# Performance work log

Measured on AMD Instinct MI355X. Metric: run time of the kernel, lower is better.

## Reference

```python
import jax, jax.numpy as jnp
import numpy as np

B, T, DM, H, D, BT = 4, 2048, 1024, 16, 64, 16
ETA_BASE = 0.01
LN_EPS = 1e-05
THETA = 10000.0


def _ln(x, w, b):
    # x: (B,H,t,D); per-head LayerNorm over last dim, w/b: (H,D)
    mu = x.mean(-1, keepdims=True)
    var = x.var(-1, keepdims=True)
    xhat = (x - mu) * jax.lax.rsqrt(var + LN_EPS)
    return xhat * w[None, :, None, :] + b[None, :, None, :]


def _ln_bwd(x, g, w):
    # gradient of LayerNorm wrt input x given upstream grad g on the output
    mu = x.mean(-1, keepdims=True)
    var = x.var(-1, keepdims=True)
    inv = jax.lax.rsqrt(var + LN_EPS)
    xhat = (x - mu) * inv
    dxhat = g * w[None, :, None, :]
    return (dxhat - dxhat.mean(-1, keepdims=True) - xhat * (dxhat * xhat).mean(-1, keepdims=True)) * inv


def _rope(q, k):
    # standard rotate-half RoPE, start_pos = 0
    pos = jnp.arange(T, dtype=jnp.float32)
    inv_freq = 1.0 / (THETA ** (jnp.arange(0, D, 2, dtype=jnp.float32) / D))
    freqs = pos[:, None] * inv_freq[None, :]            # (T, D/2)
    emb = jnp.concatenate([freqs, freqs], axis=-1)      # (T, D)
    cos = jnp.cos(emb)[None, None]                      # (1,1,T,D)
    sin = jnp.sin(emb)[None, None]

    def rot(x):
        x1, x2 = jnp.split(x, 2, axis=-1)
        return jnp.concatenate([-x2, x1], axis=-1)

    return q * cos + rot(q) * sin, k * cos + rot(k) * sin


def _forward(x, W, Wq, Wk, Wv, Wo, Wlr, ln_w, ln_b):
    def shape(y):
        return y.reshape(B, T, H, D).transpose(0, 2, 1, 3)  # (B,H,T,D)

    q = shape(x @ Wq.T)
    k = shape(x @ Wk.T)
    v = shape(x @ Wv.T)
    q, k = _rope(q, k)

    # lr gating: eta = eta_base * sigmoid(theta_lr(x)), shared across heads
    eta = ETA_BASE * jax.nn.sigmoid(x @ Wlr.T)          # (B,T,1)
    eta = jnp.broadcast_to(eta, (B, T, H)).transpose(0, 2, 1)  # (B,H,T)

    nc = T // BT

    def chunks(a):
        return a.reshape(B, H, nc, BT, D).transpose(2, 0, 1, 3, 4)  # (nc,B,H,BT,D)

    Kc, Vc, Qc = chunks(k), chunks(v), chunks(q)
    Ec = eta.reshape(B, H, nc, BT).transpose(2, 0, 1, 3)            # (nc,B,H,BT)
    mask = jnp.tril(jnp.ones((BT, BT), dtype=bool), -1)              # strict lower

    def step(Wst, inp):
        Kb, Vb, Qb, Eb = inp
        tK = jnp.einsum('bhtd,bhed->bhte', Kb, Wst)                  # K @ W^T
        g = (2.0 / BT) * (Kb + _ln(tK, ln_w, ln_b) - Vb)
        u = _ln_bwd(tK, g, ln_w)
        S = jnp.einsum('bhtd,bhsd->bhts', Qb, Kb)
        Ue = u * Eb[..., None]
        corr = jnp.einsum('bhts,bhse->bhte', jnp.where(mask, S, 0.0), Ue)
        TQ = jnp.einsum('bhtd,bhed->bhte', Qb, Wst) - corr
        Z = Qb + _ln(TQ, ln_w, ln_b)
        Wn = Wst - jnp.einsum('bhti,bhtj->bhij', Ue, Kb)
        return Wn, Z

    Wf, Zc = jax.lax.scan(step, W, (Kc, Vc, Qc, Ec))
    # (nc,B,H,BT,D) -> (B,T,H*D)
    z = Zc.transpose(1, 2, 0, 3, 4).reshape(B, H, T, D).transpose(0, 2, 1, 3).reshape(B, T, H * D)
    return z @ Wo.T, Wf


def setup_inputs() -> dict:
    key = jax.random.key(0)
    ks = jax.random.split(key, 9)
    return {
        'x': jax.random.normal(ks[0], (B, T, DM), dtype=jnp.float32),
        'W': 0.02 * jax.random.normal(ks[1], (B, H, D, D), dtype=jnp.float32),
        'Wq': 0.02 * jax.random.normal(ks[2], (DM, DM), dtype=jnp.float32),
        'Wk': 0.02 * jax.random.normal(ks[3], (DM, DM), dtype=jnp.float32),
        'Wv': 0.02 * jax.random.normal(ks[4], (DM, DM), dtype=jnp.float32),
        'Wo': 0.02 * jax.random.normal(ks[5], (DM, DM), dtype=jnp.float32),
        'Wlr': 0.02 * jax.random.normal(ks[6], (1, DM), dtype=jnp.float32),
        'ln_w': jnp.ones((H, D), dtype=jnp.float32),
        'ln_b': jnp.zeros((H, D), dtype=jnp.float32),
    }


def reference(x, W, Wq, Wk, Wv, Wo, Wlr, ln_w, ln_b):
    return _forward(x, W, Wq, Wk, Wv, Wo, Wlr, ln_w, ln_b)
```

## Files before the change

kernel.cpp:

```cpp
#include <hip/hip_runtime.h>
#include <math.h>

#define B_ 4
#define T_ 2048
#define DM_ 1024
#define H_ 16
#define D_ 64
#define BT_ 16
#define NC_ 128

typedef _Float16 half8 __attribute__((ext_vector_type(8)));
typedef _Float16 half4 __attribute__((ext_vector_type(4)));
typedef float f32x4 __attribute__((ext_vector_type(4)));

#define MFMA16 __builtin_amdgcn_mfma_f32_16x16x32_f16

__device__ __forceinline__ void stage16(const _Float16* g, _Float16* l) {
  __builtin_amdgcn_global_load_lds(
      (const __attribute__((address_space(1))) unsigned int*)(const void*)g,
      (__attribute__((address_space(3))) unsigned int*)(void*)l, 16, 0, 0);
}

template <int CTRL>
__device__ __forceinline__ float dppadd(float x) {
  return x + __int_as_float(__builtin_amdgcn_update_dpp(0, __float_as_int(x), CTRL, 0xf, 0xf, true));
}
__device__ __forceinline__ float wrs(float v) {
  v = dppadd<0x111>(v);
  v = dppadd<0x112>(v);
  v = dppadd<0x114>(v);
  v = dppadd<0x118>(v);
  v = dppadd<0x142>(v);
  v = dppadd<0x143>(v);
  return __int_as_float(__builtin_amdgcn_readlane(__float_as_int(v), 63));
}

__device__ __forceinline__ int sw128(int row, int slot) {
  return row * 128 + ((slot ^ (row & 7)) * 16);
}

__global__ void k_rope_table(float* __restrict__ cosT, float* __restrict__ sinT) {
  int idx = blockIdx.x * blockDim.x + threadIdx.x;
  if (idx >= T_ * 32) return;
  int t = idx >> 5, i = idx & 31;
  float inv = powf(10000.0f, -((float)(2 * i)) / 64.0f);
  float f = (float)t * inv;
  cosT[idx] = cosf(f);
  sinT[idx] = sinf(f);
}

__global__ __launch_bounds__(256) void k_eta(const float* __restrict__ x,
                                             const float* __restrict__ Wlr,
                                             float* __restrict__ eta) {
  int w = threadIdx.x >> 6, l = threadIdx.x & 63;
  int row = blockIdx.x * 4 + w;
  const float* xr = x + (size_t)row * DM_;
  float s = 0.f;
#pragma unroll
  for (int j = 0; j < DM_ / 64; ++j) s += xr[j * 64 + l] * Wlr[j * 64 + l];
  s = wrs(s);
  if (l == 0) eta[row] = 0.01f / (1.0f + expf(-s));
}

__global__ __launch_bounds__(256) void k_cvt(const float* __restrict__ x,
                                             const float* __restrict__ Wq,
                                             const float* __restrict__ Wk,
                                             const float* __restrict__ Wv,
                                             const float* __restrict__ Wo,
                                             _Float16* __restrict__ xh,
                                             _Float16* __restrict__ wh) {
  int gid = blockIdx.x * 256 + threadIdx.x;
  const float* src;
  _Float16* dst;
  size_t off;
  if (gid < 1048576) {
    src = x; dst = xh; off = (size_t)gid * 8;
  } else {
    int j = gid - 1048576;
    int sel = j >> 17, jj = j & 131071;
    src = (sel == 0) ? Wq : (sel == 1) ? Wk : (sel == 2) ? Wv : Wo;
    dst = wh + (size_t)sel * 1048576;
    off = (size_t)jj * 8;
  }
  float4 a = *(const float4*)&src[off];
  float4 b = *(const float4*)&src[off + 4];
  half8 h;
  h[0] = (_Float16)a.x; h[1] = (_Float16)a.y; h[2] = (_Float16)a.z; h[3] = (_Float16)a.w;
  h[4] = (_Float16)b.x; h[5] = (_Float16)b.y; h[6] = (_Float16)b.z; h[7] = (_Float16)b.w;
  *(half8*)&dst[off] = h;
}

__global__ __launch_bounds__(256) void k_gemm_qkv_h(const _Float16* __restrict__ xh,
                                                    const _Float16* __restrict__ wh,
                                                    const float* __restrict__ cosT,
                                                    const float* __restrict__ sinT,
                                                    _Float16* __restrict__ qo,
                                                    _Float16* __restrict__ ko,
                                                    _Float16* __restrict__ vo) {
  __shared__ __align__(16) union {
    _Float16 ab[2][128 * 64];
    _Float16 ep[128][136];
  } sm;
  _Float16* As = sm.ab[0];
  _Float16* Bs = sm.ab[1];
  int tid = threadIdx.x;
  int m0 = blockIdx.x * 128;
  int by = blockIdx.y;
  int mat = by >> 3;
  int n0 = (by & 7) * 128;
  const _Float16* Bsrc = wh + (size_t)mat * 1048576;
  _Float16* op = (mat == 0) ? qo : (mat == 1) ? ko : vo;
  int wid = tid >> 6, l = tid & 63;
  int m0w = (wid >> 1) * 64, n0w = (wid & 1) * 64;
  int l15 = l & 15, l4 = l >> 4;

  f32x4 acc[4][4];
#pragma unroll
  for (int i = 0; i < 4; ++i)
#pragma unroll
    for (int j = 0; j < 4; ++j) acc[i][j] = (f32x4){0.f, 0.f, 0.f, 0.f};

  int srow_in = l >> 3;
  int schunk_l = l & 7;
  for (int k0 = 0; k0 < 1024; k0 += 64) {
#pragma unroll
    for (int i = 0; i < 4; ++i) {
      int row = wid * 32 + i * 8 + srow_in;
      int sc = schunk_l ^ (row & 7);
      stage16(xh + (size_t)(m0 + row) * 1024 + k0 + sc * 8, As + (wid * 32 + i * 8) * 64);
      stage16(Bsrc + (size_t)(n0 + row) * 1024 + k0 + sc * 8, Bs + (wid * 32 + i * 8) * 64);
    }
    __syncthreads();
#pragma unroll
    for (int kk = 0; kk < 2; ++kk) {
      half8 a[4], b[4];
#pragma unroll
      for (int mi = 0; mi < 4; ++mi) {
        int row = m0w + mi * 16 + l15;
        a[mi] = *(half8*)((char*)As + sw128(row, kk * 4 + l4));
      }
#pragma unroll
      for (int ni = 0; ni < 4; ++ni) {
        int row = n0w + ni * 16 + l15;
        b[ni] = *(half8*)((char*)Bs + sw128(row, kk * 4 + l4));
      }
#pragma unroll
      for (int mi = 0; mi < 4; ++mi)
#pragma unroll
        for (int ni = 0; ni < 4; ++ni)
          acc[mi][ni] = MFMA16(a[mi], b[ni], acc[mi][ni], 0, 0, 0);
    }
    __syncthreads();
  }

  if (mat < 2) {
#pragma unroll
    for (int mi = 0; mi < 4; ++mi)
#pragma unroll
      for (int r = 0; r < 4; ++r) {
        int m = m0 + m0w + mi * 16 + l4 * 4 + r;
        int t = m & (T_ - 1);
#pragma unroll
        for (int ni = 0; ni < 2; ++ni) {
          int d1 = ni * 16 + l15;
          float cv = cosT[t * 32 + d1];
          float sv = sinT[t * 32 + d1];
          float x1 = acc[mi][ni][r], x2 = acc[mi][ni + 2][r];
          acc[mi][ni][r] = x1 * cv - x2 * sv;
          acc[mi][ni + 2][r] = x2 * cv + x1 * sv;
        }
      }
  }

#pragma unroll
  for (int mi = 0; mi < 4; ++mi)
#pragma unroll
    for (int ni = 0; ni < 4; ++ni)
#pragma unroll
      for (int r = 0; r < 4; ++r) {
        int mrow = m0w + mi * 16 + l4 * 4 + r;
        int ncol = n0w + ni * 16 + l15;
        sm.ep[mrow][ncol] = (_Float16)acc[mi][ni][r];
      }
  __syncthreads();
  int bb = m0 >> 11, t0 = m0 & (T_ - 1);
#pragma unroll
  for (int seg = 0; seg < 2; ++seg) {
    int h0 = (by & 7) * 2 + seg;
    _Float16* dsth = op + ((size_t)(bb * H_ + h0) * T_ + t0) * D_;
#pragma unroll
    for (int p = 0; p < 4; ++p) {
      int idx = p * 256 + tid;
      int mrow = idx >> 3, c = idx & 7;
      half8 hv = *(half8*)&sm.ep[mrow][seg * 64 + c * 8];
      *(half8*)&dsth[mrow * 64 + c * 8] = hv;
    }
  }
}

__global__ __launch_bounds__(256) void k_gemm_out_h(const _Float16* __restrict__ zh,
                                                    const _Float16* __restrict__ woh,
                                                    float* __restrict__ out) {
  __shared__ __align__(16) union {
    _Float16 ab[2][128 * 64];
    float epf[64][132];
  } sm;
  _Float16* As = sm.ab[0];
  _Float16* Bs = sm.ab[1];
  int tid = threadIdx.x;
  int m0 = blockIdx.x * 128;
  int n0 = blockIdx.y * 128;
  int wid = tid >> 6, l = tid & 63;
  int m0w = (wid >> 1) * 64, n0w = (wid & 1) * 64;
  int l15 = l & 15, l4 = l >> 4;

  f32x4 acc[4][4];
#pragma unroll
  for (int i = 0; i < 4; ++i)
#pragma unroll
    for (int j = 0; j < 4; ++j) acc[i][j] = (f32x4){0.f, 0.f, 0.f, 0.f};

  int srow_in = l >> 3;
  int schunk_l = l & 7;
  for (int k0 = 0; k0 < 1024; k0 += 64) {
#pragma unroll
    for (int i = 0; i < 4; ++i) {
      int row = wid * 32 + i * 8 + srow_in;
      int sc = schunk_l ^ (row & 7);
      stage16(zh + (size_t)(m0 + row) * 1024 + k0 + sc * 8, As + (wid * 32 + i * 8) * 64);
      stage16(woh + (size_t)(n0 + row) * 1024 + k0 + sc * 8, Bs + (wid * 32 + i * 8) * 64);
    }
    __syncthreads();
#pragma unroll
    for (int kk = 0; kk < 2; ++kk) {
      half8 a[4], b[4];
#pragma unroll
      for (int mi = 0; mi < 4; ++mi) {
        int row = m0w + mi * 16 + l15;
        a[mi] = *(half8*)((char*)As + sw128(row, kk * 4 + l4));
      }
#pragma unroll
      for (int ni = 0; ni < 4; ++ni) {
        int row = n0w + ni * 16 + l15;
        b[ni] = *(half8*)((char*)Bs + sw128(row, kk * 4 + l4));
      }
#pragma unroll
      for (int mi = 0; mi < 4; ++mi)
#pragma unroll
        for (int ni = 0; ni < 4; ++ni)
          acc[mi][ni] = MFMA16(a[mi], b[ni], acc[mi][ni], 0, 0, 0);
    }
    __syncthreads();
  }

#pragma unroll
  for (int hi = 0; hi < 2; ++hi) {
    if ((wid >> 1) == hi) {
#pragma unroll
      for (int mi = 0; mi < 4; ++mi)
#pragma unroll
        for (int ni = 0; ni < 4; ++ni)
#pragma unroll
          for (int r = 0; r < 4; ++r)
            sm.epf[mi * 16 + l4 * 4 + r][n0w + ni * 16 + l15] = acc[mi][ni][r];
    }
    __syncthreads();
#pragma unroll
    for (int p = 0; p < 8; ++p) {
      int idx = p * 256 + tid;
      int mrow = idx >> 5, c = idx & 31;
      float4 v = *(float4*)&sm.epf[mrow][c * 4];
      *(float4*)&out[(size_t)(m0 + hi * 64 + mrow) * DM_ + n0 + c * 4] = v;
    }
    __syncthreads();
  }
}

__global__ __launch_bounds__(512) void k_scan(const _Float16* __restrict__ qg,
                                              const _Float16* __restrict__ kg,
                                              const _Float16* __restrict__ vg,
                                              const float* __restrict__ etag,
                                              const float* __restrict__ W0,
                                              const float* __restrict__ lnw_g,
                                              const float* __restrict__ lnb_g,
                                              _Float16* __restrict__ zg,
                                              float* __restrict__ wf) {
  __shared__ __align__(16) float Ksf[2][16][68], Qsf[2][16][68], Vsf[2][16][68];
  __shared__ __align__(16) _Float16 Ks_h[2][1024], Qs_h[2][1024];
  __shared__ __align__(16) _Float16 KT_h[2][64 * 24];
  __shared__ __align__(16) _Float16 Wh[64 * 64];
  __shared__ __align__(16) float tKs[16][68], tqs[16][68];
  __shared__ __align__(16) _Float16 Ss_h[16 * 24];
  __shared__ __align__(16) _Float16 UeT_h[64 * 24];
  __shared__ float Es[2][16];

  int bh = blockIdx.x, b = bh >> 4, h = bh & 15;
  int tid = threadIdx.x, w = tid >> 6, l = tid & 63;
  int l15 = l & 15, g = l >> 4;
  int ti = w >> 1, tj0 = (w & 1) * 2, tj1 = tj0 + 1;
  int d0 = tj0 * 16 + l15, d1 = tj1 * 16 + l15;

  float lw = lnw_g[h * 64 + l];
  float lb = lnb_g[h * 64 + l];
  const _Float16* kb = kg + (size_t)bh * (T_ * D_);
  const _Float16* qb = qg + (size_t)bh * (T_ * D_);
  const _Float16* vb = vg + (size_t)bh * (T_ * D_);

  const float* w0p = W0 + (size_t)bh * 4096;
  f32x4 accW0, accW1;
#pragma unroll
  for (int r = 0; r < 4; ++r) {
    int e = ti * 16 + g * 4 + r;
    accW0[r] = w0p[e * 64 + d0];
    accW1[r] = w0p[e * 64 + d1];
  }
#pragma unroll
  for (int r = 0; r < 4; ++r) {
    int e = ti * 16 + g * 4 + r;
    *(_Float16*)((char*)Wh + sw128(e, d0 >> 3) + (d0 & 7) * 2) = (_Float16)accW0[r];
    *(_Float16*)((char*)Wh + sw128(e, d1 >> 3) + (d1 & 7) * 2) = (_Float16)accW1[r];
  }

  {
    if (tid < 256) {
      int r = tid >> 4, c4 = (tid & 15) * 4;
      half4 fk = *(const half4*)&kb[r * 64 + c4];
      half4 fv = *(const half4*)&vb[r * 64 + c4];
#pragma unroll
      for (int i = 0; i < 4; ++i) {
        Ksf[0][r][c4 + i] = (float)fk[i];
        Vsf[0][r][c4 + i] = (float)fv[i];
        *(_Float16*)((char*)KT_h[0] + (c4 + i) * 48 + r * 2) = (_Float16)(-(float)fk[i]);
      }
      *(half4*)((char*)Ks_h[0] + sw128(r, c4 >> 3) + (c4 & 7) * 2) = fk;
      if (tid < 16) Es[0][tid] = etag[b * T_ + tid];
    } else {
      int t2 = tid - 256;
      int r = t2 >> 4, c4 = (t2 & 15) * 4;
      half4 fq = *(const half4*)&qb[r * 64 + c4];
#pragma unroll
      for (int i = 0; i < 4; ++i) Qsf[0][r][c4 + i] = (float)fq[i];
      *(half4*)((char*)Qs_h[0] + sw128(r, c4 >> 3) + (c4 & 7) * 2) = fq;
    }
  }

  const half8 Z8 = {0, 0, 0, 0, 0, 0, 0, 0};

  for (int c = 0; c < NC_; ++c) {
    int cur = c & 1, nxt = cur ^ 1;
    __syncthreads();

    bool pf = (c + 1 < NC_);
    half4 fk, fv, fq;
    float fe = 0.f;
    if (pf) {
      int goff = (c + 1) * (BT_ * D_);
      if (tid < 256) {
        int r = tid >> 4, c4 = (tid & 15) * 4;
        fk = *(const half4*)&kb[goff + r * 64 + c4];
        fv = *(const half4*)&vb[goff + r * 64 + c4];
        if (tid < 16) fe = etag[b * T_ + (c + 1) * BT_ + tid];
      } else {
        int t2 = tid - 256;
        int r = t2 >> 4, c4 = (t2 & 15) * 4;
        fq = *(const half4*)&qb[goff + r * 64 + c4];
      }
    }

    int j = w & 3;
    const _Float16* Asrc = (w < 4) ? Ks_h[cur] : Qs_h[cur];
    half8 a0 = *(const half8*)((const char*)Asrc + sw128(l15, g));
    half8 a1 = *(const half8*)((const char*)Asrc + sw128(l15, 4 + g));
    int ecol = j * 16 + l15;
    half8 b0 = *(const half8*)((const char*)Wh + sw128(ecol, g));
    half8 b1 = *(const half8*)((const char*)Wh + sw128(ecol, 4 + g));
    f32x4 accA = (f32x4){0.f, 0.f, 0.f, 0.f};
    accA = MFMA16(a0, b0, accA, 0, 0, 0);
    accA = MFMA16(a1, b1, accA, 0, 0, 0);
    if (w < 4) {
#pragma unroll
      for (int r = 0; r < 4; ++r) tKs[g * 4 + r][j * 16 + l15] = accA[r];
    } else if (w == 4) {
      f32x4 accS = (f32x4){0.f, 0.f, 0.f, 0.f};
      half8 kb0 = *(const half8*)((const char*)Ks_h[cur] + sw128(l15, g));
      half8 kb1 = *(const half8*)((const char*)Ks_h[cur] + sw128(l15, 4 + g));
      accS = MFMA16(a0, kb0, accS, 0, 0, 0);
      accS = MFMA16(a1, kb1, accS, 0, 0, 0);
#pragma unroll
      for (int r = 0; r < 4; ++r) {
        int t = g * 4 + r;
        Ss_h[t * 24 + l15] = (l15 < t) ? (_Float16)(-accS[r]) : (_Float16)0.f;
      }
    }
    __syncthreads();

#pragma unroll
    for (int i = 0; i < 2; ++i) {
      int t = i * 8 + w;
      float tkv = tKs[t][l];
      float s1 = wrs(tkv);
      float s2 = wrs(tkv * tkv);
      float mu = s1 * 0.015625f;
      float var = s2 * 0.015625f - mu * mu;
      float inv = rsqrtf(var + 1e-5f);
      float xhat = (tkv - mu) * inv;
      float ln = xhat * lw + lb;
      float gg = 0.125f * (Ksf[cur][t][l] + ln - Vsf[cur][t][l]);
      float dxh = gg * lw;
      float m1 = wrs(dxh) * 0.015625f;
      float m2 = wrs(dxh * xhat) * 0.015625f;
      float ue = (dxh - m1 - xhat * m2) * inv * Es[cur][t];
      UeT_h[l * 24 + t] = (_Float16)ue;
    }
    __syncthreads();

    if (w >= 4) {
      half8 as = Z8, bu = Z8;
      if (g < 2) {
        as = *(const half8*)((const char*)Ss_h + l15 * 48 + g * 16);
        bu = *(const half8*)((const char*)UeT_h + ((w - 4) * 16 + l15) * 48 + g * 16);
      }
      accA = MFMA16(as, bu, accA, 0, 0, 0);
#pragma unroll
      for (int r = 0; r < 4; ++r) tqs[g * 4 + r][(w - 4) * 16 + l15] = accA[r];
    }
    {
      half8 au = Z8, bk0 = Z8, bk1 = Z8;
      if (g < 2) {
        au = *(const half8*)((const char*)UeT_h + (ti * 16 + l15) * 48 + g * 16);
        bk0 = *(const half8*)((const char*)KT_h[cur] + (tj0 * 16 + l15) * 48 + g * 16);
        bk1 = *(const half8*)((const char*)KT_h[cur] + (tj1 * 16 + l15) * 48 + g * 16);
      }
      accW0 = MFMA16(au, bk0, accW0, 0, 0, 0);
      accW1 = MFMA16(au, bk1, accW1, 0, 0, 0);
#pragma unroll
      for (int r = 0; r < 4; ++r) {
        int e = ti * 16 + g * 4 + r;
        *(_Float16*)((char*)Wh + sw128(e, d0 >> 3) + (d0 & 7) * 2) = (_Float16)accW0[r];
        *(_Float16*)((char*)Wh + sw128(e, d1 >> 3) + (d1 & 7) * 2) = (_Float16)accW1[r];
      }
    }
    __syncthreads();

#pragma unroll
    for (int i = 0; i < 2; ++i) {
      int t = i * 8 + w;
      float tq = tqs[t][l];
      float s1 = wrs(tq);
      float s2 = wrs(tq * tq);
      float mu = s1 * 0.015625f;
      float var = s2 * 0.015625f - mu * mu;
      float inv = rsqrtf(var + 1e-5f);
      float zv = Qsf[cur][t][l] + ((tq - mu) * inv) * lw + lb;
      zg[((size_t)(b * T_ + c * BT_ + t)) * DM_ + h * 64 + l] = (_Float16)zv;
    }
    if (pf) {
      if (tid < 256) {
        int r = tid >> 4, c4 = (tid & 15) * 4;
#pragma unroll
        for (int i = 0; i < 4; ++i) {
          Ksf[nxt][r][c4 + i] = (float)fk[i];
          Vsf[nxt][r][c4 + i] = (float)fv[i];
          *(_Float16*)((char*)KT_h[nxt] + (c4 + i) * 48 + r * 2) = (_Float16)(-(float)fk[i]);
        }
        *(half4*)((char*)Ks_h[nxt] + sw128(r, c4 >> 3) + (c4 & 7) * 2) = fk;
        if (tid < 16) Es[nxt][tid] = fe;
      } else {
        int t2 = tid - 256;
        int r = t2 >> 4, c4 = (t2 & 15) * 4;
#pragma unroll
        for (int i = 0; i < 4; ++i) Qsf[nxt][r][c4 + i] = (float)fq[i];
        *(half4*)((char*)Qs_h[nxt] + sw128(r, c4 >> 3) + (c4 & 7) * 2) = fq;
      }
    }
  }

#pragma unroll
  for (int r = 0; r < 4; ++r) {
    int e = ti * 16 + g * 4 + r;
    wf[(size_t)bh * 4096 + e * 64 + d0] = accW0[r];
    wf[(size_t)bh * 4096 + e * 64 + d1] = accW1[r];
  }
}

extern "C" void kernel_launch(void* const* d_in, const int* in_sizes, int n_in,
                              void* d_out, int out_size, void* d_ws, size_t ws_size,
                              hipStream_t stream) {
  const float* x   = (const float*)d_in[0];
  const float* W0  = (const float*)d_in[1];
  const float* Wq  = (const float*)d_in[2];
  const float* Wk  = (const float*)d_in[3];
  const float* Wv  = (const float*)d_in[4];
  const float* Wo  = (const float*)d_in[5];
  const float* Wlr = (const float*)d_in[6];
  const float* lnw = (const float*)d_in[7];
  const float* lnb = (const float*)d_in[8];
  float* out = (float*)d_out;
  float* ws = (float*)d_ws;

  float* eta  = ws;
  float* cosT = eta + 8192;
  float* sinT = cosT + 65536;
  _Float16* q  = (_Float16*)(sinT + 65536);
  _Float16* k  = q + 8388608;
  _Float16* v  = k + 8388608;
  _Float16* xh = v + 8388608;
  _Float16* wh = xh + 8388608;
  _Float16* zh = xh;
  float* wf = out + 8388608;

  hipLaunchKernelGGL(k_rope_table, dim3(256), dim3(256), 0, stream, cosT, sinT);
  hipLaunchKernelGGL(k_cvt, dim3(6144), dim3(256), 0, stream, x, Wq, Wk, Wv, Wo, xh, wh);
  hipLaunchKernelGGL(k_eta, dim3(2048), dim3(256), 0, stream, x, Wlr, eta);
  hipLaunchKernelGGL(k_gemm_qkv_h, dim3(64, 24), dim3(256), 0, stream, xh, wh, cosT, sinT, q, k, v);
  hipLaunchKernelGGL(k_scan, dim3(64), dim3(512), 0, stream, q, k, v, eta, W0, lnw, lnb, zh, wf);
  hipLaunchKernelGGL(k_gemm_out_h, dim3(64, 8), dim3(256), 0, stream, zh, wh + 3145728, out);
}
```

Measured before the change: 426.5 us.

## Specialize scan warps into K/W-update and Q-output groups with skewed pipeline

Restructures the sequential chunk scan so warps 0-3 own the W state and the K-side gradient path, while warps 4-7 handle the Q path. The Q output's final MFMA, LayerNorm and store are deferred by one chunk so they overlap the next chunk's K-side work, cutting per-chunk barriers from four to three. Next-chunk K/Q tiles are prefetched with global_load_lds into swizzled, double-buffered LDS, and the fp32 K/Q/V LDS copies are replaced by per-thread register loads. This adds an epilogue for the last chunk, more LDS double buffers, and a less balanced work split between the warp groups.

```diff
diff --git a/kernel.cpp b/kernel.cpp
--- a/kernel.cpp
+++ b/kernel.cpp
@@ -37,6 +37,9 @@
 
 __device__ __forceinline__ int sw128(int row, int slot) {
   return row * 128 + ((slot ^ (row & 7)) * 16);
+}
+__device__ __forceinline__ int p64(int row, int slot) {
+  return row * 64 + ((slot ^ ((row >> 1) & 3)) * 16);
 }
 
 __global__ void k_rope_table(float* __restrict__ cosT, float* __restrict__ sinT) {
@@ -285,20 +288,18 @@
                                               const float* __restrict__ lnb_g,
                                               _Float16* __restrict__ zg,
                                               float* __restrict__ wf) {
-  __shared__ __align__(16) float Ksf[2][16][68], Qsf[2][16][68], Vsf[2][16][68];
-  __shared__ __align__(16) _Float16 Ks_h[2][1024], Qs_h[2][1024];
-  __shared__ __align__(16) _Float16 KT_h[2][64 * 24];
-  __shared__ __align__(16) _Float16 Wh[64 * 64];
-  __shared__ __align__(16) float tKs[16][68], tqs[16][68];
-  __shared__ __align__(16) _Float16 Ss_h[16 * 24];
-  __shared__ __align__(16) _Float16 UeT_h[64 * 24];
-  __shared__ float Es[2][16];
+  __shared__ __align__(16) _Float16 Wh[4096];
+  __shared__ __align__(16) _Float16 Kh[2][1024];
+  __shared__ __align__(16) _Float16 Qh[2][1024];
+  __shared__ __align__(16) _Float16 KTl[2][2048];
+  __shared__ __align__(16) _Float16 UeTl[2][2048];
+  __shared__ __align__(16) _Float16 Ssl[2][512];
+  __shared__ float tKs[16][68];
+  __shared__ float tqs[16][68];
 
   int bh = blockIdx.x, b = bh >> 4, h = bh & 15;
   int tid = threadIdx.x, w = tid >> 6, l = tid & 63;
-  int l15 = l & 15, g = l >> 4;
-  int ti = w >> 1, tj0 = (w & 1) * 2, tj1 = tj0 + 1;
-  int d0 = tj0 * 16 + l15, d1 = tj1 * 16 + l15;
+  int l15 = l & 15, g = l >> 4, u = w - 4;
 
   float lw = lnw_g[h * 64 + l];
   float lb = lnb_g[h * 64 + l];
@@ -306,180 +307,222 @@
   const _Float16* qb = qg + (size_t)bh * (T_ * D_);
   const _Float16* vb = vg + (size_t)bh * (T_ * D_);
 
-  const float* w0p = W0 + (size_t)bh * 4096;
-  f32x4 accW0, accW1;
-#pragma unroll
-  for (int r = 0; r < 4; ++r) {
-    int e = ti * 16 + g * 4 + r;
-    accW0[r] = w0p[e * 64 + d0];
-    accW1[r] = w0p[e * 64 + d1];
-  }
-#pragma unroll
-  for (int r = 0; r < 4; ++r) {
-    int e = ti * 16 + g * 4 + r;
-    *(_Float16*)((char*)Wh + sw128(e, d0 >> 3) + (d0 & 7) * 2) = (_Float16)accW0[r];
-    *(_Float16*)((char*)Wh + sw128(e, d1 >> 3) + (d1 & 7) * 2) = (_Float16)accW1[r];
-  }
-
+  f32x4 accW[4];
+  f32x4 accQ = (f32x4){0.f, 0.f, 0.f, 0.f};
+
+  if (w < 4) {
+    const float* w0p = W0 + (size_t)bh * 4096;
+#pragma unroll
+    for (int dt = 0; dt < 4; ++dt)
+#pragma unroll
+      for (int r = 0; r < 4; ++r)
+        accW[dt][r] = w0p[(w * 16 + g * 4 + r) * 64 + dt * 16 + l15];
+#pragma unroll
+    for (int dt = 0; dt < 4; ++dt)
+#pragma unroll
+      for (int r = 0; r < 4; ++r) {
+        int e = w * 16 + g * 4 + r, d = dt * 16 + l15;
+        *(_Float16*)((char*)Wh + e * 128 + (((d >> 3) ^ (e & 7)) * 16) + (d & 7) * 2) =
+            (_Float16)accW[dt][r];
+      }
+  }
+  for (int i = tid; i < 4096; i += 512) {
+    ((_Float16*)KTl)[i] = (_Float16)0.f;
+    ((_Float16*)UeTl)[i] = (_Float16)0.f;
+  }
+  for (int i = tid; i < 1024; i += 512) ((_Float16*)Ssl)[i] = (_Float16)0.f;
+  __syncthreads();
+
+  if (w >= 4) {
+    const _Float16* src = (w < 6) ? kb : qb;
+    _Float16* dst = (w < 6) ? Kh[0] : Qh[0];
+    int hf = w & 1, row = hf * 8 + (l >> 3), ch = (l & 7) ^ (row & 7);
+    stage16(src + row * 64 + ch * 8, dst + hf * 512);
+    if (w == 4) {
+      half8 ka = *(const half8*)(kb + (l & 15) * 64 + (l >> 4) * 16);
+      half8 ka2 = *(const half8*)(kb + (l & 15) * 64 + (l >> 4) * 16 + 8);
+#pragma unroll
+      for (int i = 0; i < 16; ++i) {
+        float v = (float)((i < 8) ? ka[i] : ka2[i - 8]);
+        int d = (l >> 4) * 16 + i, t = l & 15;
+        *(_Float16*)((char*)KTl[0] + d * 64 + ((((t >> 3)) ^ ((d >> 1) & 3)) * 16) + (t & 7) * 2) =
+            (_Float16)(-v);
+      }
+    }
+  }
+
+  float kf[4], vf[4], et[4], qf[4];
+#pragma unroll
+  for (int i = 0; i < 4; ++i) { kf[i] = vf[i] = et[i] = qf[i] = 0.f; }
+
+  for (int c = 0; c < NC_; ++c) {
+    int cb = c & 1, p = cb ^ 1;
+    __syncthreads();
+
+    if (w < 4) {
+#pragma unroll
+      for (int i = 0; i < 4; ++i) {
+        int t = i * 4 + w;
+        kf[i] = (float)kb[c * 1024 + t * 64 + l];
+        vf[i] = (float)vb[c * 1024 + t * 64 + l];
+        et[i] = etag[b * T_ + c * BT_ + t];
+      }
+      half8 bw0 = *(half8*)((char*)Wh + sw128(w * 16 + l15, g));
+      half8 bw1 = *(half8*)((char*)Wh + sw128(w * 16 + l15, 4 + g));
+      half8 ak0 = *(half8*)((char*)Kh[cb] + sw128(l15, g));
+      half8 ak1 = *(half8*)((char*)Kh[cb] + sw128(l15, 4 + g));
+      f32x4 a = (f32x4){0.f, 0.f, 0.f, 0.f};
+      a = MFMA16(ak0, bw0, a, 0, 0, 0);
+      a = MFMA16(ak1, bw1, a, 0, 0, 0);
+#pragma unroll
+      for (int r = 0; r < 4; ++r) tKs[g * 4 + r][w * 16 + l15] = a[r];
+    } else {
+      if (c > 0) {
+#pragma unroll
+        for (int i = 0; i < 4; ++i) {
+          int t = i * 4 + u;
+          qf[i] = (float)qb[(c - 1) * 1024 + t * 64 + l];
+        }
+        half8 as = *(half8*)((char*)Ssl[p] + p64(l15, g));
+        half8 bu = *(half8*)((char*)UeTl[p] + p64(u * 16 + l15, g));
+        accQ = MFMA16(as, bu, accQ, 0, 0, 0);
+#pragma unroll
+        for (int r = 0; r < 4; ++r) tqs[g * 4 + r][u * 16 + l15] = accQ[r];
+      }
+    }
+    half8 kpa = {0,0,0,0,0,0,0,0}, kpb = {0,0,0,0,0,0,0,0};
+    if (w == 4 && c + 1 < NC_) {
+      kpa = *(const half8*)(kb + (size_t)(c + 1) * 1024 + (l & 15) * 64 + (l >> 4) * 16);
+      kpb = *(const half8*)(kb + (size_t)(c + 1) * 1024 + (l & 15) * 64 + (l >> 4) * 16 + 8);
+    }
+    __syncthreads();
+
+    if (w < 4) {
+#pragma unroll
+      for (int i = 0; i < 4; ++i) {
+        int t = i * 4 + w;
+        float tkv = tKs[t][l];
+        float s1 = wrs(tkv);
+        float s2 = wrs(tkv * tkv);
+        float mu = s1 * 0.015625f;
+        float var = s2 * 0.015625f - mu * mu;
+        float inv = rsqrtf(var + 1e-5f);
+        float xhat = (tkv - mu) * inv;
+        float ln = xhat * lw + lb;
+        float gg = 0.125f * (kf[i] + ln - vf[i]);
+        float dxh = gg * lw;
+        float m1 = wrs(dxh) * 0.015625f;
+        float m2 = wrs(dxh * xhat) * 0.015625f;
+        float ue = (dxh - m1 - xhat * m2) * inv * et[i];
+        *(_Float16*)((char*)UeTl[cb] + p64(l, t >> 3) + (t & 7) * 2) = (_Float16)ue;
+      }
+    } else {
+      if (c > 0) {
+#pragma unroll
+        for (int i = 0; i < 4; ++i) {
+          int t = i * 4 + u;
+          float tq = tqs[t][l];
+          float s1 = wrs(tq);
+          float s2 = wrs(tq * tq);
+          float mu = s1 * 0.015625f;
+          float var = s2 * 0.015625f - mu * mu;
+          float inv = rsqrtf(var + 1e-5f);
+          float zv = qf[i] + ((tq - mu) * inv) * lw + lb;
+          zg[((size_t)(b * T_ + (c - 1) * BT_ + t)) * DM_ + h * 64 + l] = (_Float16)zv;
+        }
+      }
+      half8 bw0 = *(half8*)((char*)Wh + sw128(u * 16 + l15, g));
+      half8 bw1 = *(half8*)((char*)Wh + sw128(u * 16 + l15, 4 + g));
+      half8 aq0 = *(half8*)((char*)Qh[cb] + sw128(l15, g));
+      half8 aq1 = *(half8*)((char*)Qh[cb] + sw128(l15, 4 + g));
+      accQ = (f32x4){0.f, 0.f, 0.f, 0.f};
+      accQ = MFMA16(aq0, bw0, accQ, 0, 0, 0);
+      accQ = MFMA16(aq1, bw1, accQ, 0, 0, 0);
+      if (w == 4) {
+        half8 bk0 = *(half8*)((char*)Kh[cb] + sw128(l15, g));
+        half8 bk1 = *(half8*)((char*)Kh[cb] + sw128(l15, 4 + g));
+        f32x4 aS = (f32x4){0.f, 0.f, 0.f, 0.f};
+        aS = MFMA16(aq0, bk0, aS, 0, 0, 0);
+        aS = MFMA16(aq1, bk1, aS, 0, 0, 0);
+#pragma unroll
+        for (int r = 0; r < 4; ++r) {
+          int t = g * 4 + r;
+          _Float16 sv = (l15 < t) ? (_Float16)(-aS[r]) : (_Float16)0.f;
+          *(_Float16*)((char*)Ssl[cb] + p64(t, l15 >> 3) + (l15 & 7) * 2) = sv;
+        }
+      }
+    }
+    __syncthreads();
+
+    if (w < 4) {
+      half8 aU = *(half8*)((char*)UeTl[cb] + p64(w * 16 + l15, g));
+#pragma unroll
+      for (int dt = 0; dt < 4; ++dt) {
+        half8 bK = *(half8*)((char*)KTl[cb] + p64(dt * 16 + l15, g));
+        accW[dt] = MFMA16(aU, bK, accW[dt], 0, 0, 0);
+      }
+#pragma unroll
+      for (int dt = 0; dt < 4; ++dt)
+#pragma unroll
+        for (int r = 0; r < 4; ++r) {
+          int e = w * 16 + g * 4 + r, d = dt * 16 + l15;
+          *(_Float16*)((char*)Wh + e * 128 + (((d >> 3) ^ (e & 7)) * 16) + (d & 7) * 2) =
+              (_Float16)accW[dt][r];
+        }
+    } else if (c + 1 < NC_) {
+      int nb = cb ^ 1;
+      const _Float16* src = (w < 6) ? kb : qb;
+      _Float16* dst = (w < 6) ? Kh[nb] : Qh[nb];
+      int hf = w & 1, row = hf * 8 + (l >> 3), ch = (l & 7) ^ (row & 7);
+      stage16(src + (size_t)(c + 1) * 1024 + row * 64 + ch * 8, dst + hf * 512);
+      if (w == 4) {
+#pragma unroll
+        for (int i = 0; i < 16; ++i) {
+          float v = (float)((i < 8) ? kpa[i] : kpb[i - 8]);
+          int d = (l >> 4) * 16 + i, t = l & 15;
+          *(_Float16*)((char*)KTl[nb] + d * 64 + ((((t >> 3)) ^ ((d >> 1) & 3)) * 16) +
+                       (t & 7) * 2) = (_Float16)(-v);
+        }
+      }
+    }
+  }
+
+  __syncthreads();
   {
-    if (tid < 256) {
-      int r = tid >> 4, c4 = (tid & 15) * 4;
-      half4 fk = *(const half4*)&kb[r * 64 + c4];
-      half4 fv = *(const half4*)&vb[r * 64 + c4];
+    int p = (NC_ - 1) & 1;
+    if (w >= 4) {
 #pragma unroll
       for (int i = 0; i < 4; ++i) {
-        Ksf[0][r][c4 + i] = (float)fk[i];
-        Vsf[0][r][c4 + i] = (float)fv[i];
-        *(_Float16*)((char*)KT_h[0] + (c4 + i) * 48 + r * 2) = (_Float16)(-(float)fk[i]);
-      }
-      *(half4*)((char*)Ks_h[0] + sw128(r, c4 >> 3) + (c4 & 7) * 2) = fk;
-      if (tid < 16) Es[0][tid] = etag[b * T_ + tid];
-    } else {
-      int t2 = tid - 256;
-      int r = t2 >> 4, c4 = (t2 & 15) * 4;
-      half4 fq = *(const half4*)&qb[r * 64 + c4];
-#pragma unroll
-      for (int i = 0; i < 4; ++i) Qsf[0][r][c4 + i] = (float)fq[i];
-      *(half4*)((char*)Qs_h[0] + sw128(r, c4 >> 3) + (c4 & 7) * 2) = fq;
-    }
-  }
-
-  const half8 Z8 = {0, 0, 0, 0, 0, 0, 0, 0};
-
-  for (int c = 0; c < NC_; ++c) {
-    int cur = c & 1, nxt = cur ^ 1;
-    __syncthreads();
-
-    bool pf = (c + 1 < NC_);
-    half4 fk, fv, fq;
-    float fe = 0.f;
-    if (pf) {
-      int goff = (c + 1) * (BT_ * D_);
-      if (tid < 256) {
-        int r = tid >> 4, c4 = (tid & 15) * 4;
-        fk = *(const half4*)&kb[goff + r * 64 + c4];
-        fv = *(const half4*)&vb[goff + r * 64 + c4];
-        if (tid < 16) fe = etag[b * T_ + (c + 1) * BT_ + tid];
-      } else {
-        int t2 = tid - 256;
-        int r = t2 >> 4, c4 = (t2 & 15) * 4;
-        fq = *(const half4*)&qb[goff + r * 64 + c4];
-      }
-    }
-
-    int j = w & 3;
-    const _Float16* Asrc = (w < 4) ? Ks_h[cur] : Qs_h[cur];
-    half8 a0 = *(const half8*)((const char*)Asrc + sw128(l15, g));
-    half8 a1 = *(const half8*)((const char*)Asrc + sw128(l15, 4 + g));
-    int ecol = j * 16 + l15;
-    half8 b0 = *(const half8*)((const char*)Wh + sw128(ecol, g));
-    half8 b1 = *(const half8*)((const char*)Wh + sw128(ecol, 4 + g));
-    f32x4 accA = (f32x4){0.f, 0.f, 0.f, 0.f};
-    accA = MFMA16(a0, b0, accA, 0, 0, 0);
-    accA = MFMA16(a1, b1, accA, 0, 0, 0);
-    if (w < 4) {
-#pragma unroll
-      for (int r = 0; r < 4; ++r) tKs[g * 4 + r][j * 16 + l15] = accA[r];
-    } else if (w == 4) {
-      f32x4 accS = (f32x4){0.f, 0.f, 0.f, 0.f};
-      half8 kb0 = *(const half8*)((const char*)Ks_h[cur] + sw128(l15, g));
-      half8 kb1 = *(const half8*)((const char*)Ks_h[cur] + sw128(l15, 4 + g));
-      accS = MFMA16(a0, kb0, accS, 0, 0, 0);
-      accS = MFMA16(a1, kb1, accS, 0, 0, 0);
-#pragma unroll
-      for (int r = 0; r < 4; ++r) {
-        int t = g * 4 + r;
-        Ss_h[t * 24 + l15] = (l15 < t) ? (_Float16)(-accS[r]) : (_Float16)0.f;
-      }
-    }
-    __syncthreads();
-
-#pragma unroll
-    for (int i = 0; i < 2; ++i) {
-      int t = i * 8 + w;
-      float tkv = tKs[t][l];
-      float s1 = wrs(tkv);
-      float s2 = wrs(tkv * tkv);
-      float mu = s1 * 0.015625f;
-      float var = s2 * 0.015625f - mu * mu;
-      float inv = rsqrtf(var + 1e-5f);
-      float xhat = (tkv - mu) * inv;
-      float ln = xhat * lw + lb;
-      float gg = 0.125f * (Ksf[cur][t][l] + ln - Vsf[cur][t][l]);
-      float dxh = gg * lw;
-      float m1 = wrs(dxh) * 0.015625f;
-      float m2 = wrs(dxh * xhat) * 0.015625f;
-      float ue = (dxh - m1 - xhat * m2) * inv * Es[cur][t];
-      UeT_h[l * 24 + t] = (_Float16)ue;
-    }
-    __syncthreads();
-
-    if (w >= 4) {
-      half8 as = Z8, bu = Z8;
-      if (g < 2) {
-        as = *(const half8*)((const char*)Ss_h + l15 * 48 + g * 16);
-        bu = *(const half8*)((const char*)UeT_h + ((w - 4) * 16 + l15) * 48 + g * 16);
-      }
-      accA = MFMA16(as, bu, accA, 0, 0, 0);
-#pragma unroll
-      for (int r = 0; r < 4; ++r) tqs[g * 4 + r][(w - 4) * 16 + l15] = accA[r];
-    }
-    {
-      half8 au = Z8, bk0 = Z8, bk1 = Z8;
-      if (g < 2) {
-        au = *(const half8*)((const char*)UeT_h + (ti * 16 + l15) * 48 + g * 16);
-        bk0 = *(const half8*)((const char*)KT_h[cur] + (tj0 * 16 + l15) * 48 + g * 16);
-        bk1 = *(const half8*)((const char*)KT_h[cur] + (tj1 * 16 + l15) * 48 + g * 16);
-      }
-      accW0 = MFMA16(au, bk0, accW0, 0, 0, 0);
-      accW1 = MFMA16(au, bk1, accW1, 0, 0, 0);
-#pragma unroll
-      for (int r = 0; r < 4; ++r) {
-        int e = ti * 16 + g * 4 + r;
-        *(_Float16*)((char*)Wh + sw128(e, d0 >> 3) + (d0 & 7) * 2) = (_Float16)accW0[r];
-        *(_Float16*)((char*)Wh + sw128(e, d1 >> 3) + (d1 & 7) * 2) = (_Float16)accW1[r];
-      }
-    }
-    __syncthreads();
-
-#pragma unroll
-    for (int i = 0; i < 2; ++i) {
-      int t = i * 8 + w;
+        int t = i * 4 + u;
+        qf[i] = (float)qb[(size_t)(NC_ - 1) * 1024 + t * 64 + l];
+      }
+      half8 as = *(half8*)((char*)Ssl[p] + p64(l15, g));
+      half8 bu = *(half8*)((char*)UeTl[p] + p64(u * 16 + l15, g));
+      accQ = MFMA16(as, bu, accQ, 0, 0, 0);
+#pragma unroll
+      for (int r = 0; r < 4; ++r) tqs[g * 4 + r][u * 16 + l15] = accQ[r];
+    }
+  }
+  __syncthreads();
+  if (w >= 4) {
+#pragma unroll
+    for (int i = 0; i < 4; ++i) {
+      int t = i * 4 + u;
       float tq = tqs[t][l];
       float s1 = wrs(tq);
       float s2 = wrs(tq * tq);
       float mu = s1 * 0.015625f;
       float var = s2 * 0.015625f - mu * mu;
       float inv = rsqrtf(var + 1e-5f);
-      float zv = Qsf[cur][t][l] + ((tq - mu) * inv) * lw + lb;
-      zg[((size_t)(b * T_ + c * BT_ + t)) * DM_ + h * 64 + l] = (_Float16)zv;
-    }
-    if (pf) {
-      if (tid < 256) {
-        int r = tid >> 4, c4 = (tid & 15) * 4;
-#pragma unroll
-        for (int i = 0; i < 4; ++i) {
-          Ksf[nxt][r][c4 + i] = (float)fk[i];
-          Vsf[nxt][r][c4 + i] = (float)fv[i];
-          *(_Float16*)((char*)KT_h[nxt] + (c4 + i) * 48 + r * 2) = (_Float16)(-(float)fk[i]);
-        }
-        *(half4*)((char*)Ks_h[nxt] + sw128(r, c4 >> 3) + (c4 & 7) * 2) = fk;
-        if (tid < 16) Es[nxt][tid] = fe;
-      } else {
-        int t2 = tid - 256;
-        int r = t2 >> 4, c4 = (t2 & 15) * 4;
-#pragma unroll
-        for (int i = 0; i < 4; ++i) Qsf[nxt][r][c4 + i] = (float)fq[i];
-        *(half4*)((char*)Qs_h[nxt] + sw128(r, c4 >> 3) + (c4 & 7) * 2) = fq;
-      }
-    }
-  }
-
-#pragma unroll
-  for (int r = 0; r < 4; ++r) {
-    int e = ti * 16 + g * 4 + r;
-    wf[(size_t)bh * 4096 + e * 64 + d0] = accW0[r];
-    wf[(size_t)bh * 4096 + e * 64 + d1] = accW1[r];
+      float zv = qf[i] + ((tq - mu) * inv) * lw + lb;
+      zg[((size_t)(b * T_ + (NC_ - 1) * BT_ + t)) * DM_ + h * 64 + l] = (_Float16)zv;
+    }
+  } else {
+#pragma unroll
+    for (int dt = 0; dt < 4; ++dt)
+#pragma unroll
+      for (int r = 0; r < 4; ++r)
+        wf[(size_t)bh * 4096 + (w * 16 + g * 4 + r) * 64 + dt * 16 + l15] = accW[dt][r];
   }
 }
 
```

Result: no change. 426.6 us (+0.0%).
